# Kernel tuning notes

Measured on AMD Instinct MI355X. Metric: run time of the kernel, lower is better.

The kernel has to match this reference:

```python
import jax, jax.numpy as jnp
import numpy as np

B = 131072
N_CONF = 512
N_REP = 256            # n_confounder_rep == n_outcome_rep
N_TREAT = 64           # 2 ** n_cause, n_cause = 6
COMBINED = 2 * N_REP   # 512


def _mlp_params(key, d_in, d_hid, d_out, scale=0.02):
    k1, k2, k3, k4 = jax.random.split(key, 4)
    return (jax.random.normal(k1, (d_hid, d_in), jnp.float32) * scale,
            jax.random.normal(k2, (d_hid,), jnp.float32) * scale,
            jax.random.normal(k3, (d_out, d_hid), jnp.float32) * scale,
            jax.random.normal(k4, (d_out,), jnp.float32) * scale)


def setup_inputs() -> dict:
    key = jax.random.key(0)
    kx, kc, k1, k2, k3, kh = jax.random.split(key, 6)
    x = jax.random.normal(kx, (B, N_CONF), jnp.float32)
    cause = jax.random.randint(kc, (B,), 0, N_TREAT, jnp.int64 if jax.config.jax_enable_x64 else jnp.int32)
    W1c, b1c, W2c, b2c = _mlp_params(k1, N_CONF, N_CONF + 1, N_REP)
    W1o, b1o, W2o, b2o = _mlp_params(k2, N_CONF, N_CONF + 1, N_REP)
    W1p, b1p, W2p, b2p = _mlp_params(k3, N_REP, N_REP + 1, N_TREAT)
    kh1, kh2 = jax.random.split(kh)
    Wh = jax.random.normal(kh1, (N_TREAT, COMBINED), jnp.float32) * 0.02  # stacked heads
    bh = jax.random.normal(kh2, (N_TREAT,), jnp.float32) * 0.02
    return {"x": x, "cause": cause,
            "W1c": W1c, "b1c": b1c, "W2c": W2c, "b2c": b2c,
            "W1o": W1o, "b1o": b1o, "W2o": W2o, "b2o": b2o,
            "W1p": W1p, "b1p": b1p, "W2p": W2p, "b2p": b2p,
            "Wh": Wh, "bh": bh}


def _mlp(x, W1, b1, W2, b2):
    h = jax.nn.relu(x @ W1.T + b1)
    return h @ W2.T + b2


def reference(x, cause, W1c, b1c, W2c, b2c, W1o, b1o, W2o, b2o,
              W1p, b1p, W2p, b2p, Wh, bh):
    confounder_rep = _mlp(x, W1c, b1c, W2c, b2c)              # [B, N_REP]
    outcome_rep = _mlp(x, W1o, b1o, W2o, b2o)                 # [B, N_REP]
    combined = jnp.concatenate([confounder_rep, outcome_rep], axis=-1)  # [B, 2*N_REP]
    # dense multi-head prediction: all N_TREAT heads, then one-hot select
    prediction = combined @ Wh.T + bh                          # [B, N_TREAT]
    cause_mat = jax.nn.one_hot(cause, N_TREAT, dtype=prediction.dtype)
    prediction_selected = jnp.sum(prediction * cause_mat, axis=1, keepdims=True)  # [B, 1]
    logits = _mlp(confounder_rep, W1p, b1p, W2p, b2p)          # [B, N_TREAT]
    log_propensity = jax.nn.log_softmax(logits, axis=-1)
    mmd = jnp.float32(0.0)  # lam_mmd == 0.0 path
    return prediction_selected, log_propensity, mmd, cause
```

## Files before the change

### kernel.cpp

```cpp
#include <hip/hip_runtime.h>


typedef __attribute__((ext_vector_type(8))) short bf16x8;
typedef __attribute__((ext_vector_type(4))) float f32x4;
typedef __attribute__((ext_vector_type(4))) short s16x4;

#define MFMA16 __builtin_amdgcn_mfma_f32_16x16x32_bf16

__device__ __forceinline__ short f2bf(float f) {
  union { float f; unsigned u; } v; v.f = f;
  return (short)((v.u + 0x7FFFu + ((v.u >> 16) & 1u)) >> 16);
}

__global__ void prep_weights(const float* __restrict__ W1c, const float* __restrict__ W2c,
                             const float* __restrict__ W1o, const float* __restrict__ W2o,
                             const float* __restrict__ W1p, const float* __restrict__ W2p,
                             const float* __restrict__ Wh,
                             const float* __restrict__ b1c, const float* __restrict__ b1o,
                             const float* __restrict__ b1p,
                             char* __restrict__ ws) {
  int s = blockIdx.x * 256 + threadIdx.x;
  if (s < 960512) {
    float v;
    if (s < 278528)      { int n = s >> 9,        k = s & 511;        v = (n < 513) ? W1c[n * 512 + k] : 0.f; }
    else if (s < 417792) { int i = s - 278528; int n = i / 544, k = i - n * 544; v = (k < 513) ? W2c[n * 513 + k] : 0.f; }
    else if (s < 696320) { int i = s - 417792; int n = i >> 9,  k = i & 511;     v = (n < 513) ? W1o[n * 512 + k] : 0.f; }
    else if (s < 835584) { int i = s - 696320; int n = i / 544, k = i - n * 544; v = (k < 513) ? W2o[n * 513 + k] : 0.f; }
    else if (s < 909312) { int i = s - 835584; int n = i >> 8,  k = i & 255;     v = (n < 257) ? W1p[n * 256 + k] : 0.f; }
    else if (s < 927744) { int i = s - 909312; int n = i / 288, k = i - n * 288; v = (k < 257) ? W2p[n * 257 + k] : 0.f; }
    else                 { v = Wh[s - 927744]; }
    ((short*)ws)[s] = f2bf(v);
  } else if (s < 961888) {
    int j = s - 960512;
    float v;
    if (j < 544)       v = (j < 513) ? b1c[j] : 0.f;
    else if (j < 1088) { int q = j - 544;  v = (q < 513) ? b1o[q] : 0.f; }
    else               { int q = j - 1088; v = (q < 257) ? b1p[q] : 0.f; }
    ((float*)(ws + 1921024))[j] = v;
  }
}

template<int NKT>
__device__ __forceinline__ void pair_mm(const short* __restrict__ W, int ldw,
                                        const short* __restrict__ A, int lda,
                                        int nt0, int l15, int l4,
                                        f32x4 (&acc0)[4], f32x4 (&acc1)[4]) {
  bf16x8 b0[NKT], b1[NKT];
  const short* w0 = W + (nt0 * 16 + l15) * ldw + l4 * 8;
  const short* w1 = w0 + 16 * ldw;
  #pragma unroll
  for (int kt = 0; kt < NKT; ++kt) {
    b0[kt] = *(const bf16x8*)(w0 + kt * 32);
    b1[kt] = *(const bf16x8*)(w1 + kt * 32);
  }
  #pragma unroll
  for (int rg = 0; rg < 4; ++rg) {
    acc0[rg] = (f32x4){0.f, 0.f, 0.f, 0.f};
    acc1[rg] = (f32x4){0.f, 0.f, 0.f, 0.f};
  }
  #pragma unroll
  for (int kt = 0; kt < NKT; ++kt) {
    #pragma unroll
    for (int rg = 0; rg < 4; ++rg) {
      bf16x8 a = *(const bf16x8*)(A + (rg * 16 + l15) * lda + kt * 32 + l4 * 8);
      acc0[rg] = MFMA16(a, b0[kt], acc0[rg], 0, 0, 0);
      acc1[rg] = MFMA16(a, b1[kt], acc1[rg], 0, 0, 0);
    }
  }
}

__device__ __forceinline__ void store_tile(short* __restrict__ dst, int ldd, int nt,
                                           const float* __restrict__ bias,
                                           const f32x4 (&acc)[4], int l15, int l4,
                                           bool relu) {
  float bi = bias[nt * 16 + l15];
  #pragma unroll
  for (int rg = 0; rg < 4; ++rg)
    #pragma unroll
    for (int r = 0; r < 4; ++r) {
      float v = acc[rg][r] + bi;
      if (relu) v = fmaxf(v, 0.f);
      dst[(rg * 16 + l4 * 4 + r) * ldd + nt * 16 + l15] = f2bf(v);
    }
}

__global__ __launch_bounds__(512, 1)
void fused_main(const float* __restrict__ x, const int* __restrict__ cause,
                const char* __restrict__ ws,
                const float* __restrict__ b2c, const float* __restrict__ b2o,
                const float* __restrict__ b2p, const float* __restrict__ bh,
                float* __restrict__ out) {
  const short* W1cb = (const short*)(ws);
  const short* W2cb = (const short*)(ws + 557056);
  const short* W1ob = (const short*)(ws + 835584);
  const short* W2ob = (const short*)(ws + 1392640);
  const short* W1pb = (const short*)(ws + 1671168);
  const short* W2pb = (const short*)(ws + 1818624);
  const short* Whb  = (const short*)(ws + 1855488);
  const float* b1cp = (const float*)(ws + 1921024);
  const float* b1op = (const float*)(ws + 1923200);
  const float* b1pp = (const float*)(ws + 1925376);

  extern __shared__ __align__(16) char lds[];
  short* Cs    = (short*)lds;
  short* Os    = (short*)(lds + 33792);
  short* Hs    = (short*)(lds + 67584);
  short* Xs    = (short*)lds;
  float* headB = (float*)(lds + 67584);
  short* Hp    = (short*)(lds + 67584);

  const int tid  = threadIdx.x;
  const int lane = tid & 63;
  const int wid  = tid >> 6;
  const int l15  = lane & 15;
  const int l4   = lane >> 4;
  const size_t grow0 = (size_t)blockIdx.x * 64;

  {
    const f32x4* xsrc = (const f32x4*)(x + grow0 * 512);
    for (int i = tid; i < 8192; i += 512) {
      f32x4 v = __builtin_nontemporal_load(xsrc + i);
      int r = i >> 7, c = i & 127;
      s16x4 p;
      p.x = f2bf(v.x); p.y = f2bf(v.y); p.z = f2bf(v.z); p.w = f2bf(v.w);
      *(s16x4*)&Xs[r * 520 + c * 4] = p;
    }
  }
  __syncthreads();

  for (int p = wid; p < 17; p += 8) {
    f32x4 a0[4], a1[4];
    pair_mm<16>(W1cb, 512, Xs, 520, 2 * p, l15, l4, a0, a1);
    store_tile(Hs, 552, 2 * p,     b1cp, a0, l15, l4, true);
    store_tile(Hs, 552, 2 * p + 1, b1cp, a1, l15, l4, true);
  }
  __syncthreads();

  s16x4 crp[2][4];
  {
    f32x4 a0[4], a1[4];
    pair_mm<17>(W2cb, 544, Hs, 552, 2 * wid, l15, l4, a0, a1);
    float bi0 = b2c[wid * 32 + l15], bi1 = b2c[wid * 32 + 16 + l15];
    #pragma unroll
    for (int rg = 0; rg < 4; ++rg) {
      s16x4 q0, q1;
      #pragma unroll
      for (int r = 0; r < 4; ++r) {
        q0[r] = f2bf(a0[rg][r] + bi0);
        q1[r] = f2bf(a1[rg][r] + bi1);
      }
      crp[0][rg] = q0; crp[1][rg] = q1;
    }
  }
  __syncthreads();

  for (int p = wid; p < 17; p += 8) {
    f32x4 a0[4], a1[4];
    pair_mm<16>(W1ob, 512, Xs, 520, 2 * p, l15, l4, a0, a1);
    store_tile(Hs, 552, 2 * p,     b1op, a0, l15, l4, true);
    store_tile(Hs, 552, 2 * p + 1, b1op, a1, l15, l4, true);
  }
  __syncthreads();

  #pragma unroll
  for (int jj = 0; jj < 2; ++jj) {
    int nt = 2 * wid + jj;
    #pragma unroll
    for (int rg = 0; rg < 4; ++rg)
      #pragma unroll
      for (int r = 0; r < 4; ++r)
        Cs[(rg * 16 + l4 * 4 + r) * 264 + nt * 16 + l15] = crp[jj][rg][r];
  }

  {
    f32x4 a0[4], a1[4];
    pair_mm<17>(W2ob, 544, Hs, 552, 2 * wid, l15, l4, a0, a1);
    store_tile(Os, 264, 2 * wid,     b2o, a0, l15, l4, false);
    store_tile(Os, 264, 2 * wid + 1, b2o, a1, l15, l4, false);
  }
  __syncthreads();

  {
    const int g = wid >> 1;
    const int rb = g * 16;
    const int ntb = (wid & 1) * 2;
    bf16x8 acf[16];
    #pragma unroll
    for (int kt = 0; kt < 8; ++kt) {
      acf[kt]     = *(const bf16x8*)&Cs[(rb + l15) * 264 + kt * 32 + l4 * 8];
      acf[kt + 8] = *(const bf16x8*)&Os[(rb + l15) * 264 + kt * 32 + l4 * 8];
    }
    f32x4 hacc[2] = {{0.f,0.f,0.f,0.f},{0.f,0.f,0.f,0.f}};
    #pragma unroll
    for (int j = 0; j < 2; ++j) {
      const short* w0 = Whb + ((ntb + j) * 16 + l15) * 512 + l4 * 8;
      #pragma unroll
      for (int kt = 0; kt < 16; ++kt)
        hacc[j] = MFMA16(acf[kt], *(const bf16x8*)(w0 + kt * 32), hacc[j], 0, 0, 0);
    }
    #pragma unroll
    for (int j = 0; j < 2; ++j)
      #pragma unroll
      for (int r = 0; r < 4; ++r)
        headB[(rb + l4 * 4 + r) * 68 + (ntb + j) * 16 + l15] = hacc[j][r];
  }
  __syncthreads();

  if (wid < 4 && lane < 16) {
    int row = wid * 16 + lane;
    size_t gr = grow0 + row;
    int cv = cause[gr];
    out[gr] = headB[row * 68 + cv] + bh[cv];
    out[(size_t)8519681 + gr] = (float)cv;
  }
  __syncthreads();

  for (int p = wid; p < 9; p += 8) {
    f32x4 a0[4], a1[4];
    pair_mm<8>(W1pb, 256, Cs, 264, 2 * p, l15, l4, a0, a1);
    store_tile(Hp, 296, 2 * p,     b1pp, a0, l15, l4, true);
    store_tile(Hp, 296, 2 * p + 1, b1pp, a1, l15, l4, true);
  }
  __syncthreads();

  if (wid < 4) {
    const int rb = wid * 16;
    f32x4 pl[4];
    {
      bf16x8 ahp[9];
      #pragma unroll
      for (int kt = 0; kt < 9; ++kt)
        ahp[kt] = *(const bf16x8*)&Hp[(rb + l15) * 296 + kt * 32 + l4 * 8];
      #pragma unroll
      for (int nt = 0; nt < 4; ++nt) {
        f32x4 a0 = {0.f, 0.f, 0.f, 0.f};
        const short* w0 = W2pb + (nt * 16 + l15) * 288 + l4 * 8;
        #pragma unroll
        for (int kt = 0; kt < 9; ++kt)
          a0 = MFMA16(ahp[kt], *(const bf16x8*)(w0 + kt * 32), a0, 0, 0, 0);
        float bi = b2p[nt * 16 + l15];
        #pragma unroll
        for (int r = 0; r < 4; ++r) a0[r] += bi;
        pl[nt] = a0;
      }
    }
    #pragma unroll
    for (int r = 0; r < 4; ++r) {
      float m = fmaxf(fmaxf(pl[0][r], pl[1][r]), fmaxf(pl[2][r], pl[3][r]));
      m = fmaxf(m, __shfl_xor(m, 1, 64));
      m = fmaxf(m, __shfl_xor(m, 2, 64));
      m = fmaxf(m, __shfl_xor(m, 4, 64));
      m = fmaxf(m, __shfl_xor(m, 8, 64));
      float s = __expf(pl[0][r] - m) + __expf(pl[1][r] - m)
              + __expf(pl[2][r] - m) + __expf(pl[3][r] - m);
      s += __shfl_xor(s, 1, 64);
      s += __shfl_xor(s, 2, 64);
      s += __shfl_xor(s, 4, 64);
      s += __shfl_xor(s, 8, 64);
      float lse = m + __logf(s);
      size_t gr = grow0 + rb + l4 * 4 + r;
      float* o1 = out + 131072 + gr * 64;
      #pragma unroll
      for (int nt = 0; nt < 4; ++nt)
        o1[nt * 16 + l15] = pl[nt][r] - lse;
    }
  }
  if (blockIdx.x == 0 && tid == 0) out[8519680] = 0.0f;
}

extern "C" void kernel_launch(void* const* d_in, const int* in_sizes, int n_in,
                              void* d_out, int out_size, void* d_ws, size_t ws_size,
                              hipStream_t stream) {
  (void)in_sizes; (void)n_in; (void)out_size; (void)ws_size;
  const float* x    = (const float*)d_in[0];
  const int*   cause= (const int*)  d_in[1];
  const float* W1c  = (const float*)d_in[2];
  const float* b1c  = (const float*)d_in[3];
  const float* W2c  = (const float*)d_in[4];
  const float* b2c  = (const float*)d_in[5];
  const float* W1o  = (const float*)d_in[6];
  const float* b1o  = (const float*)d_in[7];
  const float* W2o  = (const float*)d_in[8];
  const float* b2o  = (const float*)d_in[9];
  const float* W1p  = (const float*)d_in[10];
  const float* b1p  = (const float*)d_in[11];
  const float* W2p  = (const float*)d_in[12];
  const float* b2p  = (const float*)d_in[13];
  const float* Wh   = (const float*)d_in[14];
  const float* bh   = (const float*)d_in[15];
  char* ws = (char*)d_ws;

  prep_weights<<<3758, 256, 0, stream>>>(W1c, W2c, W1o, W2o, W1p, W2p, Wh,
                                         b1c, b1o, b1p, ws);

  (void)hipFuncSetAttribute((const void*)fused_main,
                            hipFuncAttributeMaxDynamicSharedMemorySize, 138240);
  fused_main<<<2048, 512, 138240, stream>>>(x, cause, ws, b2c, b2o, b2p, bh,
                                            (float*)d_out);
}
```

Baseline: 568.4 us.

## Double block to 1024 threads and redistribute MLP tiles across sixteen waves

Raises the fused kernel's block size from 8 to 16 waves and rewrites the work split. The second-layer GEMMs are divided by row-group halves, the head GEMM gives one N-tile per wave, and the first-layer confounder and outcome passes are assigned to different wave subsets. This is meant to add latency hiding and MFMA parallelism per CU, since only one 512-thread block fits in LDS. In exchange the register budget per thread is halved under the new launch bounds, which risks spills, and some phases leave waves idle.

```diff
diff --git a/kernel.cpp b/kernel.cpp
--- a/kernel.cpp
+++ b/kernel.cpp
@@ -40,11 +40,11 @@
   }
 }
 
-template<int NKT>
+template<int NKT, int NRG>
 __device__ __forceinline__ void pair_mm(const short* __restrict__ W, int ldw,
                                         const short* __restrict__ A, int lda,
-                                        int nt0, int l15, int l4,
-                                        f32x4 (&acc0)[4], f32x4 (&acc1)[4]) {
+                                        int nt0, int rg0, int l15, int l4,
+                                        f32x4 (&acc0)[NRG], f32x4 (&acc1)[NRG]) {
   bf16x8 b0[NKT], b1[NKT];
   const short* w0 = W + (nt0 * 16 + l15) * ldw + l4 * 8;
   const short* w1 = w0 + 16 * ldw;
@@ -54,37 +54,38 @@
     b1[kt] = *(const bf16x8*)(w1 + kt * 32);
   }
   #pragma unroll
-  for (int rg = 0; rg < 4; ++rg) {
-    acc0[rg] = (f32x4){0.f, 0.f, 0.f, 0.f};
-    acc1[rg] = (f32x4){0.f, 0.f, 0.f, 0.f};
+  for (int g = 0; g < NRG; ++g) {
+    acc0[g] = (f32x4){0.f, 0.f, 0.f, 0.f};
+    acc1[g] = (f32x4){0.f, 0.f, 0.f, 0.f};
   }
   #pragma unroll
   for (int kt = 0; kt < NKT; ++kt) {
     #pragma unroll
-    for (int rg = 0; rg < 4; ++rg) {
-      bf16x8 a = *(const bf16x8*)(A + (rg * 16 + l15) * lda + kt * 32 + l4 * 8);
-      acc0[rg] = MFMA16(a, b0[kt], acc0[rg], 0, 0, 0);
-      acc1[rg] = MFMA16(a, b1[kt], acc1[rg], 0, 0, 0);
-    }
-  }
-}
-
+    for (int g = 0; g < NRG; ++g) {
+      bf16x8 a = *(const bf16x8*)(A + ((rg0 + g) * 16 + l15) * lda + kt * 32 + l4 * 8);
+      acc0[g] = MFMA16(a, b0[kt], acc0[g], 0, 0, 0);
+      acc1[g] = MFMA16(a, b1[kt], acc1[g], 0, 0, 0);
+    }
+  }
+}
+
+template<int NRG>
 __device__ __forceinline__ void store_tile(short* __restrict__ dst, int ldd, int nt,
                                            const float* __restrict__ bias,
-                                           const f32x4 (&acc)[4], int l15, int l4,
-                                           bool relu) {
+                                           const f32x4 (&acc)[NRG], int rg0,
+                                           int l15, int l4, bool relu) {
   float bi = bias[nt * 16 + l15];
   #pragma unroll
-  for (int rg = 0; rg < 4; ++rg)
+  for (int g = 0; g < NRG; ++g)
     #pragma unroll
     for (int r = 0; r < 4; ++r) {
-      float v = acc[rg][r] + bi;
+      float v = acc[g][r] + bi;
       if (relu) v = fmaxf(v, 0.f);
-      dst[(rg * 16 + l4 * 4 + r) * ldd + nt * 16 + l15] = f2bf(v);
-    }
-}
-
-__global__ __launch_bounds__(512, 1)
+      dst[((rg0 + g) * 16 + l4 * 4 + r) * ldd + nt * 16 + l15] = f2bf(v);
+    }
+}
+
+__global__ __launch_bounds__(1024, 4)
 void fused_main(const float* __restrict__ x, const int* __restrict__ cause,
                 const char* __restrict__ ws,
                 const float* __restrict__ b2c, const float* __restrict__ b2o,
@@ -118,7 +119,7 @@
 
   {
     const f32x4* xsrc = (const f32x4*)(x + grow0 * 512);
-    for (int i = tid; i < 8192; i += 512) {
+    for (int i = tid; i < 8192; i += 1024) {
       f32x4 v = __builtin_nontemporal_load(xsrc + i);
       int r = i >> 7, c = i & 127;
       s16x4 p;
@@ -128,81 +129,78 @@
   }
   __syncthreads();
 
-  for (int p = wid; p < 17; p += 8) {
+  for (int p = wid; p < 17; p += 16) {
     f32x4 a0[4], a1[4];
-    pair_mm<16>(W1cb, 512, Xs, 520, 2 * p, l15, l4, a0, a1);
-    store_tile(Hs, 552, 2 * p,     b1cp, a0, l15, l4, true);
-    store_tile(Hs, 552, 2 * p + 1, b1cp, a1, l15, l4, true);
-  }
-  __syncthreads();
-
-  s16x4 crp[2][4];
-  {
+    pair_mm<16, 4>(W1cb, 512, Xs, 520, 2 * p, 0, l15, l4, a0, a1);
+    store_tile<4>(Hs, 552, 2 * p,     b1cp, a0, 0, l15, l4, true);
+    store_tile<4>(Hs, 552, 2 * p + 1, b1cp, a1, 0, l15, l4, true);
+  }
+  __syncthreads();
+
+  const int p2 = wid >> 1;
+  const int h2 = (wid & 1) * 2;
+  s16x4 crp[2][2];
+  {
+    f32x4 a0[2], a1[2];
+    pair_mm<17, 2>(W2cb, 544, Hs, 552, 2 * p2, h2, l15, l4, a0, a1);
+    float bi0 = b2c[p2 * 32 + l15], bi1 = b2c[p2 * 32 + 16 + l15];
+    #pragma unroll
+    for (int g = 0; g < 2; ++g) {
+      s16x4 q0, q1;
+      #pragma unroll
+      for (int r = 0; r < 4; ++r) {
+        q0[r] = f2bf(a0[g][r] + bi0);
+        q1[r] = f2bf(a1[g][r] + bi1);
+      }
+      crp[0][g] = q0; crp[1][g] = q1;
+    }
+  }
+  __syncthreads();
+
+  for (int p = (wid + 8) & 15; p < 17; p += 16) {
     f32x4 a0[4], a1[4];
-    pair_mm<17>(W2cb, 544, Hs, 552, 2 * wid, l15, l4, a0, a1);
-    float bi0 = b2c[wid * 32 + l15], bi1 = b2c[wid * 32 + 16 + l15];
-    #pragma unroll
-    for (int rg = 0; rg < 4; ++rg) {
-      s16x4 q0, q1;
-      #pragma unroll
-      for (int r = 0; r < 4; ++r) {
-        q0[r] = f2bf(a0[rg][r] + bi0);
-        q1[r] = f2bf(a1[rg][r] + bi1);
-      }
-      crp[0][rg] = q0; crp[1][rg] = q1;
-    }
-  }
-  __syncthreads();
-
-  for (int p = wid; p < 17; p += 8) {
-    f32x4 a0[4], a1[4];
-    pair_mm<16>(W1ob, 512, Xs, 520, 2 * p, l15, l4, a0, a1);
-    store_tile(Hs, 552, 2 * p,     b1op, a0, l15, l4, true);
-    store_tile(Hs, 552, 2 * p + 1, b1op, a1, l15, l4, true);
+    pair_mm<16, 4>(W1ob, 512, Xs, 520, 2 * p, 0, l15, l4, a0, a1);
+    store_tile<4>(Hs, 552, 2 * p,     b1op, a0, 0, l15, l4, true);
+    store_tile<4>(Hs, 552, 2 * p + 1, b1op, a1, 0, l15, l4, true);
   }
   __syncthreads();
 
   #pragma unroll
   for (int jj = 0; jj < 2; ++jj) {
-    int nt = 2 * wid + jj;
-    #pragma unroll
-    for (int rg = 0; rg < 4; ++rg)
+    int nt = 2 * p2 + jj;
+    #pragma unroll
+    for (int g = 0; g < 2; ++g)
       #pragma unroll
       for (int r = 0; r < 4; ++r)
-        Cs[(rg * 16 + l4 * 4 + r) * 264 + nt * 16 + l15] = crp[jj][rg][r];
-  }
-
-  {
-    f32x4 a0[4], a1[4];
-    pair_mm<17>(W2ob, 544, Hs, 552, 2 * wid, l15, l4, a0, a1);
-    store_tile(Os, 264, 2 * wid,     b2o, a0, l15, l4, false);
-    store_tile(Os, 264, 2 * wid + 1, b2o, a1, l15, l4, false);
-  }
-  __syncthreads();
-
-  {
-    const int g = wid >> 1;
+        Cs[((h2 + g) * 16 + l4 * 4 + r) * 264 + nt * 16 + l15] = crp[jj][g][r];
+  }
+
+  {
+    f32x4 a0[2], a1[2];
+    pair_mm<17, 2>(W2ob, 544, Hs, 552, 2 * p2, h2, l15, l4, a0, a1);
+    store_tile<2>(Os, 264, 2 * p2,     b2o, a0, h2, l15, l4, false);
+    store_tile<2>(Os, 264, 2 * p2 + 1, b2o, a1, h2, l15, l4, false);
+  }
+  __syncthreads();
+
+  {
+    const int g  = wid >> 2;
+    const int j  = wid & 3;
     const int rb = g * 16;
-    const int ntb = (wid & 1) * 2;
     bf16x8 acf[16];
     #pragma unroll
     for (int kt = 0; kt < 8; ++kt) {
       acf[kt]     = *(const bf16x8*)&Cs[(rb + l15) * 264 + kt * 32 + l4 * 8];
       acf[kt + 8] = *(const bf16x8*)&Os[(rb + l15) * 264 + kt * 32 + l4 * 8];
     }
-    f32x4 hacc[2] = {{0.f,0.f,0.f,0.f},{0.f,0.f,0.f,0.f}};
-    #pragma unroll
-    for (int j = 0; j < 2; ++j) {
-      const short* w0 = Whb + ((ntb + j) * 16 + l15) * 512 + l4 * 8;
-      #pragma unroll
-      for (int kt = 0; kt < 16; ++kt)
-        hacc[j] = MFMA16(acf[kt], *(const bf16x8*)(w0 + kt * 32), hacc[j], 0, 0, 0);
-    }
-    #pragma unroll
-    for (int j = 0; j < 2; ++j)
-      #pragma unroll
-      for (int r = 0; r < 4; ++r)
-        headB[(rb + l4 * 4 + r) * 68 + (ntb + j) * 16 + l15] = hacc[j][r];
+    f32x4 hacc = {0.f, 0.f, 0.f, 0.f};
+    const short* w0 = Whb + (j * 16 + l15) * 512 + l4 * 8;
+    #pragma unroll
+    for (int kt = 0; kt < 16; ++kt)
+      hacc = MFMA16(acf[kt], *(const bf16x8*)(w0 + kt * 32), hacc, 0, 0, 0);
+    #pragma unroll
+    for (int r = 0; r < 4; ++r)
+      headB[(rb + l4 * 4 + r) * 68 + j * 16 + l15] = hacc[r];
   }
   __syncthreads();
 
@@ -215,11 +213,12 @@
   }
   __syncthreads();
 
-  for (int p = wid; p < 9; p += 8) {
-    f32x4 a0[4], a1[4];
-    pair_mm<8>(W1pb, 256, Cs, 264, 2 * p, l15, l4, a0, a1);
-    store_tile(Hp, 296, 2 * p,     b1pp, a0, l15, l4, true);
-    store_tile(Hp, 296, 2 * p + 1, b1pp, a1, l15, l4, true);
+  for (int q = (wid + 4) & 15; q < 18; q += 16) {
+    int pp = q >> 1, hh = (q & 1) * 2;
+    f32x4 a0[2], a1[2];
+    pair_mm<8, 2>(W1pb, 256, Cs, 264, 2 * pp, hh, l15, l4, a0, a1);
+    store_tile<2>(Hp, 296, 2 * pp,     b1pp, a0, hh, l15, l4, true);
+    store_tile<2>(Hp, 296, 2 * pp + 1, b1pp, a1, hh, l15, l4, true);
   }
   __syncthreads();
 
@@ -295,6 +294,6 @@
 
   (void)hipFuncSetAttribute((const void*)fused_main,
                             hipFuncAttributeMaxDynamicSharedMemorySize, 138240);
-  fused_main<<<2048, 512, 138240, stream>>>(x, cause, ws, b2c, b2o, b2p, bh,
-                                            (float*)d_out);
-}
+  fused_main<<<2048, 1024, 138240, stream>>>(x, cause, ws, b2c, b2o, b2p, bh,
+                                             (float*)d_out);
+}
```

After: 640.1 us. 12.6% more time.

## Swizzle LDS tiles with XOR layout and stream weight fragments per k-step

Applied to the files above, without the earlier changes.

Replaces padded LDS row strides with an XOR-swizzled layout (8-element group index XORed with row&7) for the X, hidden, confounder/outcome and propensity-hidden tiles. The aim is to avoid LDS bank conflicts on the 16-byte MFMA operand reads and on the scattered bf16 stores. pair_mm now loads weight fragments per k-step instead of preloading all of them into registers, which lowers register pressure but exposes global/L2 latency inside the loop. The outcome-layer loop also reverses its wave assignment order, and total LDS rises slightly.

```diff
diff --git a/kernel.cpp b/kernel.cpp
--- a/kernel.cpp
+++ b/kernel.cpp
@@ -10,6 +10,14 @@
 __device__ __forceinline__ short f2bf(float f) {
   union { float f; unsigned u; } v; v.f = f;
   return (short)((v.u + 0x7FFFu + ((v.u >> 16) & 1u)) >> 16);
+}
+
+__device__ __forceinline__ const bf16x8* ldsRd8(const short* base, int row,
+                                                int grp, int LD) {
+  return (const bf16x8*)(base + row * LD + ((grp ^ (row & 7)) << 3));
+}
+__device__ __forceinline__ short* ldsPtr(short* base, int row, int col, int LD) {
+  return base + row * LD + ((((col >> 3) ^ (row & 7)) << 3) | (col & 7));
 }
 
 __global__ void prep_weights(const float* __restrict__ W1c, const float* __restrict__ W2c,
@@ -45,26 +53,22 @@
                                         const short* __restrict__ A, int lda,
                                         int nt0, int l15, int l4,
                                         f32x4 (&acc0)[4], f32x4 (&acc1)[4]) {
-  bf16x8 b0[NKT], b1[NKT];
   const short* w0 = W + (nt0 * 16 + l15) * ldw + l4 * 8;
   const short* w1 = w0 + 16 * ldw;
   #pragma unroll
-  for (int kt = 0; kt < NKT; ++kt) {
-    b0[kt] = *(const bf16x8*)(w0 + kt * 32);
-    b1[kt] = *(const bf16x8*)(w1 + kt * 32);
-  }
-  #pragma unroll
-  for (int rg = 0; rg < 4; ++rg) {
-    acc0[rg] = (f32x4){0.f, 0.f, 0.f, 0.f};
-    acc1[rg] = (f32x4){0.f, 0.f, 0.f, 0.f};
+  for (int g = 0; g < 4; ++g) {
+    acc0[g] = (f32x4){0.f, 0.f, 0.f, 0.f};
+    acc1[g] = (f32x4){0.f, 0.f, 0.f, 0.f};
   }
   #pragma unroll
   for (int kt = 0; kt < NKT; ++kt) {
-    #pragma unroll
-    for (int rg = 0; rg < 4; ++rg) {
-      bf16x8 a = *(const bf16x8*)(A + (rg * 16 + l15) * lda + kt * 32 + l4 * 8);
-      acc0[rg] = MFMA16(a, b0[kt], acc0[rg], 0, 0, 0);
-      acc1[rg] = MFMA16(a, b1[kt], acc1[rg], 0, 0, 0);
+    bf16x8 b0 = *(const bf16x8*)(w0 + kt * 32);
+    bf16x8 b1 = *(const bf16x8*)(w1 + kt * 32);
+    #pragma unroll
+    for (int g = 0; g < 4; ++g) {
+      bf16x8 a = *ldsRd8(A, g * 16 + l15, kt * 4 + l4, lda);
+      acc0[g] = MFMA16(a, b0, acc0[g], 0, 0, 0);
+      acc1[g] = MFMA16(a, b1, acc1[g], 0, 0, 0);
     }
   }
 }
@@ -75,12 +79,12 @@
                                            bool relu) {
   float bi = bias[nt * 16 + l15];
   #pragma unroll
-  for (int rg = 0; rg < 4; ++rg)
+  for (int g = 0; g < 4; ++g)
     #pragma unroll
     for (int r = 0; r < 4; ++r) {
-      float v = acc[rg][r] + bi;
+      float v = acc[g][r] + bi;
       if (relu) v = fmaxf(v, 0.f);
-      dst[(rg * 16 + l4 * 4 + r) * ldd + nt * 16 + l15] = f2bf(v);
+      *ldsPtr(dst, g * 16 + l4 * 4 + r, nt * 16 + l15, ldd) = f2bf(v);
     }
 }
 
@@ -103,11 +107,11 @@
 
   extern __shared__ __align__(16) char lds[];
   short* Cs    = (short*)lds;
-  short* Os    = (short*)(lds + 33792);
-  short* Hs    = (short*)(lds + 67584);
+  short* Os    = (short*)(lds + 32768);
+  short* Hs    = (short*)(lds + 65536);
   short* Xs    = (short*)lds;
-  float* headB = (float*)(lds + 67584);
-  short* Hp    = (short*)(lds + 67584);
+  float* headB = (float*)(lds + 65536);
+  short* Hp    = (short*)(lds + 65536);
 
   const int tid  = threadIdx.x;
   const int lane = tid & 63;
@@ -123,42 +127,43 @@
       int r = i >> 7, c = i & 127;
       s16x4 p;
       p.x = f2bf(v.x); p.y = f2bf(v.y); p.z = f2bf(v.z); p.w = f2bf(v.w);
-      *(s16x4*)&Xs[r * 520 + c * 4] = p;
+      int grp = (c >> 1) ^ (r & 7);
+      *(s16x4*)(Xs + r * 512 + (grp << 3) + ((c & 1) << 2)) = p;
     }
   }
   __syncthreads();
 
   for (int p = wid; p < 17; p += 8) {
     f32x4 a0[4], a1[4];
-    pair_mm<16>(W1cb, 512, Xs, 520, 2 * p, l15, l4, a0, a1);
-    store_tile(Hs, 552, 2 * p,     b1cp, a0, l15, l4, true);
-    store_tile(Hs, 552, 2 * p + 1, b1cp, a1, l15, l4, true);
+    pair_mm<16>(W1cb, 512, Xs, 512, 2 * p, l15, l4, a0, a1);
+    store_tile(Hs, 576, 2 * p,     b1cp, a0, l15, l4, true);
+    store_tile(Hs, 576, 2 * p + 1, b1cp, a1, l15, l4, true);
   }
   __syncthreads();
 
   s16x4 crp[2][4];
   {
     f32x4 a0[4], a1[4];
-    pair_mm<17>(W2cb, 544, Hs, 552, 2 * wid, l15, l4, a0, a1);
+    pair_mm<17>(W2cb, 544, Hs, 576, 2 * wid, l15, l4, a0, a1);
     float bi0 = b2c[wid * 32 + l15], bi1 = b2c[wid * 32 + 16 + l15];
     #pragma unroll
-    for (int rg = 0; rg < 4; ++rg) {
+    for (int g = 0; g < 4; ++g) {
       s16x4 q0, q1;
       #pragma unroll
       for (int r = 0; r < 4; ++r) {
-        q0[r] = f2bf(a0[rg][r] + bi0);
-        q1[r] = f2bf(a1[rg][r] + bi1);
+        q0[r] = f2bf(a0[g][r] + bi0);
+        q1[r] = f2bf(a1[g][r] + bi1);
       }
-      crp[0][rg] = q0; crp[1][rg] = q1;
-    }
-  }
-  __syncthreads();
-
-  for (int p = wid; p < 17; p += 8) {
-    f32x4 a0[4], a1[4];
-    pair_mm<16>(W1ob, 512, Xs, 520, 2 * p, l15, l4, a0, a1);
-    store_tile(Hs, 552, 2 * p,     b1op, a0, l15, l4, true);
-    store_tile(Hs, 552, 2 * p + 1, b1op, a1, l15, l4, true);
+      crp[0][g] = q0; crp[1][g] = q1;
+    }
+  }
+  __syncthreads();
+
+  for (int p = 7 - wid; p < 17; p += 8) {
+    f32x4 a0[4], a1[4];
+    pair_mm<16>(W1ob, 512, Xs, 512, 2 * p, l15, l4, a0, a1);
+    store_tile(Hs, 576, 2 * p,     b1op, a0, l15, l4, true);
+    store_tile(Hs, 576, 2 * p + 1, b1op, a1, l15, l4, true);
   }
   __syncthreads();
 
@@ -166,17 +171,17 @@
   for (int jj = 0; jj < 2; ++jj) {
     int nt = 2 * wid + jj;
     #pragma unroll
-    for (int rg = 0; rg < 4; ++rg)
+    for (int g = 0; g < 4; ++g)
       #pragma unroll
       for (int r = 0; r < 4; ++r)
-        Cs[(rg * 16 + l4 * 4 + r) * 264 + nt * 16 + l15] = crp[jj][rg][r];
+        *ldsPtr(Cs, g * 16 + l4 * 4 + r, nt * 16 + l15, 256) = crp[jj][g][r];
   }
 
   {
     f32x4 a0[4], a1[4];
-    pair_mm<17>(W2ob, 544, Hs, 552, 2 * wid, l15, l4, a0, a1);
-    store_tile(Os, 264, 2 * wid,     b2o, a0, l15, l4, false);
-    store_tile(Os, 264, 2 * wid + 1, b2o, a1, l15, l4, false);
+    pair_mm<17>(W2ob, 544, Hs, 576, 2 * wid, l15, l4, a0, a1);
+    store_tile(Os, 256, 2 * wid,     b2o, a0, l15, l4, false);
+    store_tile(Os, 256, 2 * wid + 1, b2o, a1, l15, l4, false);
   }
   __syncthreads();
 
@@ -187,8 +192,8 @@
     bf16x8 acf[16];
     #pragma unroll
     for (int kt = 0; kt < 8; ++kt) {
-      acf[kt]     = *(const bf16x8*)&Cs[(rb + l15) * 264 + kt * 32 + l4 * 8];
-      acf[kt + 8] = *(const bf16x8*)&Os[(rb + l15) * 264 + kt * 32 + l4 * 8];
+      acf[kt]     = *ldsRd8(Cs, rb + l15, kt * 4 + l4, 256);
+      acf[kt + 8] = *ldsRd8(Os, rb + l15, kt * 4 + l4, 256);
     }
     f32x4 hacc[2] = {{0.f,0.f,0.f,0.f},{0.f,0.f,0.f,0.f}};
     #pragma unroll
@@ -217,9 +222,9 @@
 
   for (int p = wid; p < 9; p += 8) {
     f32x4 a0[4], a1[4];
-    pair_mm<8>(W1pb, 256, Cs, 264, 2 * p, l15, l4, a0, a1);
-    store_tile(Hp, 296, 2 * p,     b1pp, a0, l15, l4, true);
-    store_tile(Hp, 296, 2 * p + 1, b1pp, a1, l15, l4, true);
+    pair_mm<8>(W1pb, 256, Cs, 256, 2 * p, l15, l4, a0, a1);
+    store_tile(Hp, 320, 2 * p,     b1pp, a0, l15, l4, true);
+    store_tile(Hp, 320, 2 * p + 1, b1pp, a1, l15, l4, true);
   }
   __syncthreads();
 
@@ -230,7 +235,7 @@
       bf16x8 ahp[9];
       #pragma unroll
       for (int kt = 0; kt < 9; ++kt)
-        ahp[kt] = *(const bf16x8*)&Hp[(rb + l15) * 296 + kt * 32 + l4 * 8];
+        ahp[kt] = *ldsRd8(Hp, rb + l15, kt * 4 + l4, 320);
       #pragma unroll
       for (int nt = 0; nt < 4; ++nt) {
         f32x4 a0 = {0.f, 0.f, 0.f, 0.f};
@@ -294,7 +299,7 @@
                                          b1c, b1o, b1p, ws);
 
   (void)hipFuncSetAttribute((const void*)fused_main,
-                            hipFuncAttributeMaxDynamicSharedMemorySize, 138240);
-  fused_main<<<2048, 512, 138240, stream>>>(x, cause, ws, b2c, b2o, b2p, bh,
+                            hipFuncAttributeMaxDynamicSharedMemorySize, 139264);
+  fused_main<<<2048, 512, 139264, stream>>>(x, cause, ws, b2c, b2o, b2p, bh,
                                             (float*)d_out);
 }
```

Result: no change. 577.1 us (+1.5%).
